# Optimization experiments

Hardware: AMD Instinct MI355X
Metric: run time of the kernel (lower is better)

## Reference

```python
import jax, jax.numpy as jnp
import numpy as np

LOSS_WEIGHT = 1.0
INTENSITY_WEIGHT = 0.5


def setup_inputs() -> dict:
    key = jax.random.key(0)
    k1, k2 = jax.random.split(key)
    N, M = 20000, 20000
    adv_pc = jax.random.normal(k1, (N, 4), dtype=jnp.float32)
    ori_pc = jax.random.normal(k2, (M, 4), dtype=jnp.float32)
    return {"adv_pc": adv_pc, "ori_pc": ori_pc}


def reference(adv_pc, ori_pc):
    adv_xyz = adv_pc[:, :3]  # [N,3]
    ori_xyz = ori_pc[:, :3]  # [M,3]

    # Squared pairwise distances via |a|^2 + |b|^2 - 2 a.b  -> [N,M]
    a2 = jnp.sum(adv_xyz * adv_xyz, axis=1)  # [N]
    b2 = jnp.sum(ori_xyz * ori_xyz, axis=1)  # [M]
    d2 = a2[:, None] + b2[None, :] - 2.0 * (adv_xyz @ ori_xyz.T)

    # 1-NN in both directions (knn_points with K=1 returns squared dists)
    min_dist_adv_to_ori = jnp.min(d2, axis=1)     # [N]
    adv_indices = jnp.argmin(d2, axis=1)          # [N] nearest ori for each adv
    min_dist_ori_to_adv = jnp.min(d2, axis=0)     # [M]
    ori_indices = jnp.argmin(d2, axis=0)          # [M] nearest adv for each ori

    chamfer_loss = jnp.mean(min_dist_adv_to_ori) + jnp.mean(min_dist_ori_to_adv)

    adv_intensity = adv_pc[:, 3]
    ori_intensity = ori_pc[:, 3]
    adv_intensity_diff_1 = jnp.mean((adv_intensity - ori_intensity[adv_indices]) ** 2)
    adv_intensity_diff_2 = jnp.mean((ori_intensity - adv_intensity[ori_indices]) ** 2)
    intensity_loss = (adv_intensity_diff_1 + adv_intensity_diff_2) / 2.0

    return chamfer_loss * LOSS_WEIGHT + intensity_loss * INTENSITY_WEIGHT
```

## Files before the change

### kernel.cpp

```cpp
#include <hip/hip_runtime.h>

#define CH 512
#define TPCH 16
#define QPB 256
#define YSL 8
#define RB 64

typedef __bf16 bf16x8 __attribute__((ext_vector_type(8)));
typedef float f32x16 __attribute__((ext_vector_type(16)));

__device__ __forceinline__ unsigned bfb(float x) {
    __bf16 h = (__bf16)x;
    return (unsigned)__builtin_bit_cast(unsigned short, h);
}
__device__ __forceinline__ float bff(unsigned b) {
    return (float)__builtin_bit_cast(__bf16, (unsigned short)b);
}

__device__ __forceinline__ void stage_one(uint4* a_lds, int local, float4 p, bool valid) {
    float x, y, z, u;
    if (valid) {
        x = p.x; y = p.y; z = p.z;
        u = 0.25f * fmaf(p.x, p.x, fmaf(p.y, p.y, p.z * p.z));
    } else {
        x = 0.f; y = 0.f; z = 0.f; u = 130.f;
    }
    unsigned xh = bfb(x); unsigned xl = bfb(x - bff(xh));
    unsigned yh = bfb(y); unsigned yl = bfb(y - bff(yh));
    unsigned zh = bfb(z); unsigned zl = bfb(z - bff(zh));
    unsigned uh = bfb(u); float u1 = u - bff(uh);
    unsigned ul = bfb(u1); unsigned ull = bfb(u1 - bff(ul));
    uint4 h0, h1;
    h0.x = xh | (xl << 16); h0.y = h0.x;
    h0.z = yh | (yl << 16); h0.w = h0.z;
    h1.x = zh | (zl << 16); h1.y = h1.x;
    h1.z = uh | (ul << 16);
    h1.w = ull | (0x43A0u << 16);
    int t = local >> 5, r = local & 31;
    a_lds[t * 64 + r]      = h0;
    a_lds[t * 64 + 32 + r] = h1;
}

__device__ __forceinline__ bf16x8 make_bfrag(float4 qp, int h) {
    float cx = -0.5f * qp.x, cy = -0.5f * qp.y, cz = -0.5f * qp.z;
    unsigned cxh = bfb(cx); unsigned cxl = bfb(cx - bff(cxh));
    unsigned cyh = bfb(cy); unsigned cyl = bfb(cy - bff(cyh));
    unsigned czh = bfb(cz); unsigned czl = bfb(cz - bff(czh));
    uint4 braw;
    if (h == 0) {
        braw.x = cxh | (cxh << 16); braw.y = cxl | (cxl << 16);
        braw.z = cyh | (cyh << 16); braw.w = cyl | (cyl << 16);
    } else {
        braw.x = czh | (czh << 16); braw.y = czl | (czl << 16);
        braw.z = 0x3F803F80u;       braw.w = 0x3F803F80u;
    }
    return __builtin_bit_cast(bf16x8, braw);
}

__device__ __forceinline__ void reduce_fold(const f32x16& acc, unsigned tl, unsigned& cm) {
    unsigned u0 = min(min(__float_as_uint(acc[0]),  __float_as_uint(acc[1])),  __float_as_uint(acc[2]));
    unsigned u1 = min(min(__float_as_uint(acc[3]),  __float_as_uint(acc[4])),  __float_as_uint(acc[5]));
    unsigned u2 = min(min(__float_as_uint(acc[6]),  __float_as_uint(acc[7])),  __float_as_uint(acc[8]));
    unsigned u3 = min(min(__float_as_uint(acc[9]),  __float_as_uint(acc[10])), __float_as_uint(acc[11]));
    unsigned u4 = min(min(__float_as_uint(acc[12]), __float_as_uint(acc[13])), __float_as_uint(acc[14]));
    unsigned u5 = min(min(u0, u1), u2);
    unsigned u6 = min(min(u3, u4), __float_as_uint(acc[15]));
    unsigned m  = min(u5, u6);
    cm = min(cm, (m << 9) | tl);
}

__global__ __launch_bounds__(256, 4) void mfma_nn(
    const float4* __restrict__ adv, int N,
    const float4* __restrict__ ori, int M,
    unsigned long long* __restrict__ slots, int S,
    int chunks)
{
    const int dir = blockIdx.z;
    const float4* __restrict__ q = dir ? ori : adv;
    const float4* __restrict__ t = dir ? adv : ori;
    const int nq = dir ? M : N;
    const int nt = dir ? N : M;
    unsigned long long* __restrict__ outrow =
        slots + (size_t)(dir * YSL + blockIdx.y) * (size_t)S;

    const int tid = threadIdx.x;
    const int wave = tid >> 6;
    const int lane = tid & 63;
    const int col = lane & 31;
    const int h = lane >> 5;

    const int qiA = blockIdx.x * QPB + wave * 32 + col;
    const int qiB = qiA + 128;
    const bool qvA = qiA < nq;
    const bool qvB = qiB < nq;
    float4 qpA = qvA ? q[qiA] : make_float4(0.f, 0.f, 0.f, 0.f);
    float4 qpB = qvB ? q[qiB] : make_float4(0.f, 0.f, 0.f, 0.f);

    const bf16x8 bfragA = make_bfrag(qpA, h);
    const bf16x8 bfragB = make_bfrag(qpB, h);

    __shared__ uint4 a_lds[TPCH * 64];
    const f32x16 zero = {};

    const int slicebase = blockIdx.y * chunks * CH;
    unsigned cmA = 0xFFFFFFFFu;
    unsigned cmB = 0xFFFFFFFFu;
    int base = slicebase;

    for (int c = 0; c < chunks; ++c) {
        if (c) __syncthreads();
        {
            int j0 = base + tid, j1 = j0 + 256;
            if (base + CH <= nt) {
                stage_one(a_lds, tid,       t[j0], true);
                stage_one(a_lds, tid + 256, t[j1], true);
            } else {
                bool v0 = j0 < nt, v1 = j1 < nt;
                float4 p0 = v0 ? t[j0] : make_float4(0.f, 0.f, 0.f, 0.f);
                float4 p1 = v1 ? t[j1] : make_float4(0.f, 0.f, 0.f, 0.f);
                stage_one(a_lds, tid,       p0, v0);
                stage_one(a_lds, tid + 256, p1, v1);
            }
        }
        __syncthreads();

        const unsigned tl0 = (unsigned)(c << 4);
        #pragma unroll
        for (int tt = 0; tt < TPCH; ++tt) {
            bf16x8 a = __builtin_bit_cast(bf16x8, a_lds[tt * 64 + lane]);
            f32x16 acc0 = __builtin_amdgcn_mfma_f32_32x32x16_bf16(a, bfragA, zero, 0, 0, 0);
            reduce_fold(acc0, tl0 + (unsigned)tt, cmA);
            f32x16 acc1 = __builtin_amdgcn_mfma_f32_32x32x16_bf16(a, bfragB, zero, 0, 0, 0);
            reduce_fold(acc1, tl0 + (unsigned)tt, cmB);
        }
        base += CH;
    }

    #pragma unroll
    for (int s = 0; s < 2; ++s) {
        const unsigned cm = s ? cmB : cmA;
        const float4 qp  = s ? qpB : qpA;
        const int    qi  = s ? qiB : qiA;
        const bool   qv  = s ? qvB : qvA;
        const int jb = slicebase + (int)(cm & 0x7Fu) * 32 + 4 * h;
        unsigned long long run = 0xFFFFFFFFFFFFFFFFull;
        #pragma unroll
        for (int e = 0; e < 16; ++e) {
            int r = (e & 3) + ((e >> 2) << 3);
            int j = jb + r;
            if (j < nt) {
                float4 b = t[j];
                float dx = qp.x - b.x, dy = qp.y - b.y, dz = qp.z - b.z;
                float d2 = fmaf(dx, dx, fmaf(dy, dy, dz * dz));
                unsigned long long cand =
                    ((unsigned long long)__float_as_uint(d2) << 32) | (unsigned)j;
                run = cand < run ? cand : run;
            }
        }
        unsigned long long other = __shfl_xor(run, 32);
        run = run < other ? run : other;
        if (h == 0 && qv) outrow[qi] = run;
    }
}

__device__ inline float block_reduce_sum(float v, float* lds) {
    #pragma unroll
    for (int off = 32; off > 0; off >>= 1) v += __shfl_down(v, off, 64);
    int wave = threadIdx.x >> 6;
    int lane = threadIdx.x & 63;
    __syncthreads();
    if (lane == 0) lds[wave] = v;
    __syncthreads();
    float r = 0.f;
    if (threadIdx.x == 0) {
        #pragma unroll
        for (int w = 0; w < 4; ++w) r += lds[w];
    }
    return r;
}

__global__ __launch_bounds__(256) void partial_finalize(
    const unsigned long long* __restrict__ slots, int S,
    int n, int m,
    const float4* __restrict__ adv, const float4* __restrict__ ori,
    float* __restrict__ partials)
{
    __shared__ float lds[4];
    float s_min0 = 0.f, s_i1 = 0.f, s_min1 = 0.f, s_i2 = 0.f;
    const int stride = RB * 256;
    const int t0 = blockIdx.x * 256 + threadIdx.x;
    const unsigned long long* __restrict__ s0 = slots;
    const unsigned long long* __restrict__ s1 = slots + (size_t)YSL * S;

    for (int i = t0; i < n; i += stride) {
        unsigned long long k = s0[i];
        #pragma unroll
        for (int y = 1; y < YSL; ++y) k = min(k, s0[(size_t)y * S + i]);
        int j = (int)(unsigned int)(k & 0xFFFFFFFFu);
        s_min0 += __uint_as_float((unsigned int)(k >> 32));
        float dw = adv[i].w - ori[j].w;
        s_i1 += dw * dw;
    }
    for (int jj = t0; jj < m; jj += stride) {
        unsigned long long k = s1[jj];
        #pragma unroll
        for (int y = 1; y < YSL; ++y) k = min(k, s1[(size_t)y * S + jj]);
        int i = (int)(unsigned int)(k & 0xFFFFFFFFu);
        s_min1 += __uint_as_float((unsigned int)(k >> 32));
        float dw = ori[jj].w - adv[i].w;
        s_i2 += dw * dw;
    }

    float r0 = block_reduce_sum(s_min0, lds);
    float r1 = block_reduce_sum(s_i1, lds);
    float r2 = block_reduce_sum(s_min1, lds);
    float r3 = block_reduce_sum(s_i2, lds);

    if (threadIdx.x == 0) {
        partials[blockIdx.x * 4 + 0] = r0;
        partials[blockIdx.x * 4 + 1] = r1;
        partials[blockIdx.x * 4 + 2] = r2;
        partials[blockIdx.x * 4 + 3] = r3;
    }
}

__global__ __launch_bounds__(256) void combine(
    const float* __restrict__ partials, int n, int m, float* __restrict__ out)
{
    __shared__ float lds[4];
    float v0 = 0.f, v1 = 0.f, v2 = 0.f, v3 = 0.f;
    if (threadIdx.x < RB) {
        v0 = partials[threadIdx.x * 4 + 0];
        v1 = partials[threadIdx.x * 4 + 1];
        v2 = partials[threadIdx.x * 4 + 2];
        v3 = partials[threadIdx.x * 4 + 3];
    }
    float r0 = block_reduce_sum(v0, lds);
    float r1 = block_reduce_sum(v1, lds);
    float r2 = block_reduce_sum(v2, lds);
    float r3 = block_reduce_sum(v3, lds);
    if (threadIdx.x == 0) {
        float chamfer   = r0 / (float)n + r2 / (float)m;
        float intensity = 0.5f * (r1 / (float)n + r3 / (float)m);
        out[0] = chamfer * 1.0f + intensity * 0.5f;
    }
}

extern "C" void kernel_launch(void* const* d_in, const int* in_sizes, int n_in,
                              void* d_out, int out_size, void* d_ws, size_t ws_size,
                              hipStream_t stream) {
    const float4* adv = (const float4*)d_in[0];
    const float4* ori = (const float4*)d_in[1];
    const int N = in_sizes[0] / 4;
    const int M = in_sizes[1] / 4;
    const int S = max(N, M);

    unsigned long long* slots = (unsigned long long*)d_ws;
    float* partials = (float*)(slots + (size_t)2 * YSL * S);
    float* out = (float*)d_out;

    const int chunks = (S + YSL * CH - 1) / (YSL * CH);
    dim3 grid((S + QPB - 1) / QPB, YSL, 2);
    mfma_nn<<<grid, 256, 0, stream>>>(adv, N, ori, M, slots, S, chunks);

    partial_finalize<<<RB, 256, 0, stream>>>(slots, S, N, M, adv, ori, partials);
    combine<<<1, 256, 0, stream>>>(partials, N, M, out);
}
```

Baseline: 47.32 us.

## Precompute bf16 split fragments in a prep kernel and stream them from global memory

Adds a prep kernel that converts both point clouds once into the hi/lo bf16 MFMA A-fragment layout in workspace. The main kernel then loads each fragment straight from global memory (L2-resident) per lane, with no LDS staging and no __syncthreads. This removes the per-block redundant conversion work and the barriers between chunks. In exchange it adds one extra kernel launch, extra workspace, and puts global load latency directly in the MFMA loop, with only an unroll of 4 to hide it.

New measurement: 62.76 us. +32.6%, slower.

```diff
diff --git a/kernel.cpp b/kernel.cpp
--- a/kernel.cpp
+++ b/kernel.cpp
@@ -1,7 +1,6 @@
 #include <hip/hip_runtime.h>
 
 #define CH 512
-#define TPCH 16
 #define QPB 256
 #define YSL 8
 #define RB 64
@@ -17,7 +16,7 @@
     return (float)__builtin_bit_cast(__bf16, (unsigned short)b);
 }
 
-__device__ __forceinline__ void stage_one(uint4* a_lds, int local, float4 p, bool valid) {
+__device__ __forceinline__ void make_frag(float4 p, bool valid, uint4& h0, uint4& h1) {
     float x, y, z, u;
     if (valid) {
         x = p.x; y = p.y; z = p.z;
@@ -30,15 +29,30 @@
     unsigned zh = bfb(z); unsigned zl = bfb(z - bff(zh));
     unsigned uh = bfb(u); float u1 = u - bff(uh);
     unsigned ul = bfb(u1); unsigned ull = bfb(u1 - bff(ul));
-    uint4 h0, h1;
     h0.x = xh | (xl << 16); h0.y = h0.x;
     h0.z = yh | (yl << 16); h0.w = h0.z;
     h1.x = zh | (zl << 16); h1.y = h1.x;
     h1.z = uh | (ul << 16);
     h1.w = ull | (0x43A0u << 16);
-    int t = local >> 5, r = local & 31;
-    a_lds[t * 64 + r]      = h0;
-    a_lds[t * 64 + 32 + r] = h1;
+}
+
+__global__ __launch_bounds__(256) void prep(
+    const float4* __restrict__ adv, int N,
+    const float4* __restrict__ ori, int M,
+    uint4* __restrict__ frag0,
+    uint4* __restrict__ frag1,
+    int padded)
+{
+    int p = blockIdx.x * 256 + threadIdx.x;
+    if (p >= padded) return;
+    int base = (p >> 5) * 64 + (p & 31);
+    uint4 h0, h1;
+    bool v0 = p < M;
+    make_frag(v0 ? ori[p] : make_float4(0.f,0.f,0.f,0.f), v0, h0, h1);
+    frag0[base] = h0; frag0[base + 32] = h1;
+    bool v1 = p < N;
+    make_frag(v1 ? adv[p] : make_float4(0.f,0.f,0.f,0.f), v1, h0, h1);
+    frag1[base] = h0; frag1[base + 32] = h1;
 }
 
 __device__ __forceinline__ bf16x8 make_bfrag(float4 qp, int h) {
@@ -72,14 +86,17 @@
 __global__ __launch_bounds__(256, 4) void mfma_nn(
     const float4* __restrict__ adv, int N,
     const float4* __restrict__ ori, int M,
+    const uint4* __restrict__ frag0,
+    const uint4* __restrict__ frag1,
     unsigned long long* __restrict__ slots, int S,
-    int chunks)
+    int ntiles)
 {
     const int dir = blockIdx.z;
     const float4* __restrict__ q = dir ? ori : adv;
     const float4* __restrict__ t = dir ? adv : ori;
     const int nq = dir ? M : N;
     const int nt = dir ? N : M;
+    const uint4* __restrict__ frag = dir ? frag1 : frag0;
     unsigned long long* __restrict__ outrow =
         slots + (size_t)(dir * YSL + blockIdx.y) * (size_t)S;
 
@@ -98,42 +115,21 @@
 
     const bf16x8 bfragA = make_bfrag(qpA, h);
     const bf16x8 bfragB = make_bfrag(qpB, h);
-
-    __shared__ uint4 a_lds[TPCH * 64];
     const f32x16 zero = {};
 
-    const int slicebase = blockIdx.y * chunks * CH;
+    const int slicebase = blockIdx.y * ntiles * 32;
+    const uint4* __restrict__ fr = frag + (size_t)(slicebase >> 5) * 64 + lane;
+
     unsigned cmA = 0xFFFFFFFFu;
     unsigned cmB = 0xFFFFFFFFu;
-    int base = slicebase;
-
-    for (int c = 0; c < chunks; ++c) {
-        if (c) __syncthreads();
-        {
-            int j0 = base + tid, j1 = j0 + 256;
-            if (base + CH <= nt) {
-                stage_one(a_lds, tid,       t[j0], true);
-                stage_one(a_lds, tid + 256, t[j1], true);
-            } else {
-                bool v0 = j0 < nt, v1 = j1 < nt;
-                float4 p0 = v0 ? t[j0] : make_float4(0.f, 0.f, 0.f, 0.f);
-                float4 p1 = v1 ? t[j1] : make_float4(0.f, 0.f, 0.f, 0.f);
-                stage_one(a_lds, tid,       p0, v0);
-                stage_one(a_lds, tid + 256, p1, v1);
-            }
-        }
-        __syncthreads();
-
-        const unsigned tl0 = (unsigned)(c << 4);
-        #pragma unroll
-        for (int tt = 0; tt < TPCH; ++tt) {
-            bf16x8 a = __builtin_bit_cast(bf16x8, a_lds[tt * 64 + lane]);
-            f32x16 acc0 = __builtin_amdgcn_mfma_f32_32x32x16_bf16(a, bfragA, zero, 0, 0, 0);
-            reduce_fold(acc0, tl0 + (unsigned)tt, cmA);
-            f32x16 acc1 = __builtin_amdgcn_mfma_f32_32x32x16_bf16(a, bfragB, zero, 0, 0, 0);
-            reduce_fold(acc1, tl0 + (unsigned)tt, cmB);
-        }
-        base += CH;
+
+    #pragma unroll 4
+    for (int tl = 0; tl < ntiles; ++tl) {
+        bf16x8 a = __builtin_bit_cast(bf16x8, fr[(size_t)tl * 64]);
+        f32x16 acc0 = __builtin_amdgcn_mfma_f32_32x32x16_bf16(a, bfragA, zero, 0, 0, 0);
+        reduce_fold(acc0, (unsigned)tl, cmA);
+        f32x16 acc1 = __builtin_amdgcn_mfma_f32_32x32x16_bf16(a, bfragB, zero, 0, 0, 0);
+        reduce_fold(acc1, (unsigned)tl, cmB);
     }
 
     #pragma unroll
@@ -255,13 +251,20 @@
     const int M = in_sizes[1] / 4;
     const int S = max(N, M);
 
+    const int chunks = (S + YSL * CH - 1) / (YSL * CH);
+    const int ntiles = chunks * (CH / 32);
+    const int padded = YSL * ntiles * 32;
+
     unsigned long long* slots = (unsigned long long*)d_ws;
-    float* partials = (float*)(slots + (size_t)2 * YSL * S);
+    uint4* frag0 = (uint4*)(slots + (size_t)2 * YSL * S);
+    uint4* frag1 = frag0 + (size_t)padded * 2;
+    float* partials = (float*)(frag1 + (size_t)padded * 2);
     float* out = (float*)d_out;
 
-    const int chunks = (S + YSL * CH - 1) / (YSL * CH);
+    prep<<<(padded + 255) / 256, 256, 0, stream>>>(adv, N, ori, M, frag0, frag1, padded);
+
     dim3 grid((S + QPB - 1) / QPB, YSL, 2);
-    mfma_nn<<<grid, 256, 0, stream>>>(adv, N, ori, M, slots, S, chunks);
+    mfma_nn<<<grid, 256, 0, stream>>>(adv, N, ori, M, frag0, frag1, slots, S, ntiles);
 
     partial_finalize<<<RB, 256, 0, stream>>>(slots, S, N, M, adv, ori, partials);
     combine<<<1, 256, 0, stream>>>(partials, N, M, out);
```

## Stage targets per wave in private LDS and block four query groups per lane

Applied to the files above, without the earlier changes.

Each wave now loads and converts its own 256-target chunk into a private LDS region, which removes the block-wide __syncthreads between staging and MFMA use. Each lane also holds four query fragments instead of two, and the block covers 512 queries, so each loaded A fragment feeds four MFMAs. In exchange, every wave redundantly loads and converts the same targets, so conversion work per MFMA roughly doubles. Register pressure also rises and the grid has half as many blocks, which may lower occupancy.

Result: slower. 61.65 us (+30.3%).

```diff
diff --git a/kernel.cpp b/kernel.cpp
--- a/kernel.cpp
+++ b/kernel.cpp
@@ -1,8 +1,8 @@
 #include <hip/hip_runtime.h>
 
-#define CH 512
-#define TPCH 16
-#define QPB 256
+#define WCH 256
+#define WTPC 8
+#define QPB 512
 #define YSL 8
 #define RB 64
 
@@ -17,7 +17,7 @@
     return (float)__builtin_bit_cast(__bf16, (unsigned short)b);
 }
 
-__device__ __forceinline__ void stage_one(uint4* a_lds, int local, float4 p, bool valid) {
+__device__ __forceinline__ void make_frag(float4 p, bool valid, uint4& h0, uint4& h1) {
     float x, y, z, u;
     if (valid) {
         x = p.x; y = p.y; z = p.z;
@@ -30,15 +30,11 @@
     unsigned zh = bfb(z); unsigned zl = bfb(z - bff(zh));
     unsigned uh = bfb(u); float u1 = u - bff(uh);
     unsigned ul = bfb(u1); unsigned ull = bfb(u1 - bff(ul));
-    uint4 h0, h1;
     h0.x = xh | (xl << 16); h0.y = h0.x;
     h0.z = yh | (yl << 16); h0.w = h0.z;
     h1.x = zh | (zl << 16); h1.y = h1.x;
     h1.z = uh | (ul << 16);
     h1.w = ull | (0x43A0u << 16);
-    int t = local >> 5, r = local & 31;
-    a_lds[t * 64 + r]      = h0;
-    a_lds[t * 64 + 32 + r] = h1;
 }
 
 __device__ __forceinline__ bf16x8 make_bfrag(float4 qp, int h) {
@@ -73,7 +69,7 @@
     const float4* __restrict__ adv, int N,
     const float4* __restrict__ ori, int M,
     unsigned long long* __restrict__ slots, int S,
-    int chunks)
+    int wchunks)
 {
     const int dir = blockIdx.z;
     const float4* __restrict__ q = dir ? ori : adv;
@@ -89,59 +85,61 @@
     const int col = lane & 31;
     const int h = lane >> 5;
 
-    const int qiA = blockIdx.x * QPB + wave * 32 + col;
-    const int qiB = qiA + 128;
-    const bool qvA = qiA < nq;
-    const bool qvB = qiB < nq;
-    float4 qpA = qvA ? q[qiA] : make_float4(0.f, 0.f, 0.f, 0.f);
-    float4 qpB = qvB ? q[qiB] : make_float4(0.f, 0.f, 0.f, 0.f);
-
-    const bf16x8 bfragA = make_bfrag(qpA, h);
-    const bf16x8 bfragB = make_bfrag(qpB, h);
-
-    __shared__ uint4 a_lds[TPCH * 64];
+    const int qi0 = blockIdx.x * QPB + wave * 32 + col;
+    float4 qp[4]; bool qv[4]; bf16x8 bfrag[4];
+    #pragma unroll
+    for (int s = 0; s < 4; ++s) {
+        int qi = qi0 + s * 128;
+        qv[s] = qi < nq;
+        qp[s] = qv[s] ? q[qi] : make_float4(0.f, 0.f, 0.f, 0.f);
+        bfrag[s] = make_bfrag(qp[s], h);
+    }
     const f32x16 zero = {};
 
-    const int slicebase = blockIdx.y * chunks * CH;
-    unsigned cmA = 0xFFFFFFFFu;
-    unsigned cmB = 0xFFFFFFFFu;
+    __shared__ uint4 lds_all[4][WTPC * 64];
+    uint4* my_lds = lds_all[wave];
+
+    const int slicebase = blockIdx.y * wchunks * WCH;
+    unsigned cm0 = 0xFFFFFFFFu, cm1 = 0xFFFFFFFFu;
+    unsigned cm2 = 0xFFFFFFFFu, cm3 = 0xFFFFFFFFu;
     int base = slicebase;
 
-    for (int c = 0; c < chunks; ++c) {
-        if (c) __syncthreads();
+    for (int c = 0; c < wchunks; ++c) {
         {
-            int j0 = base + tid, j1 = j0 + 256;
-            if (base + CH <= nt) {
-                stage_one(a_lds, tid,       t[j0], true);
-                stage_one(a_lds, tid + 256, t[j1], true);
-            } else {
-                bool v0 = j0 < nt, v1 = j1 < nt;
-                float4 p0 = v0 ? t[j0] : make_float4(0.f, 0.f, 0.f, 0.f);
-                float4 p1 = v1 ? t[j1] : make_float4(0.f, 0.f, 0.f, 0.f);
-                stage_one(a_lds, tid,       p0, v0);
-                stage_one(a_lds, tid + 256, p1, v1);
+            bool full = (base + WCH <= nt);
+            #pragma unroll
+            for (int k = 0; k < 4; ++k) {
+                int j = base + k * 64 + lane;
+                bool v = full || (j < nt);
+                float4 p = v ? t[j] : make_float4(0.f, 0.f, 0.f, 0.f);
+                uint4 h0, h1;
+                make_frag(p, v, h0, h1);
+                int local = k * 64 + lane;
+                int tl = local >> 5, r = local & 31;
+                my_lds[tl * 64 + r]      = h0;
+                my_lds[tl * 64 + 32 + r] = h1;
             }
         }
-        __syncthreads();
-
-        const unsigned tl0 = (unsigned)(c << 4);
-        #pragma unroll
-        for (int tt = 0; tt < TPCH; ++tt) {
-            bf16x8 a = __builtin_bit_cast(bf16x8, a_lds[tt * 64 + lane]);
-            f32x16 acc0 = __builtin_amdgcn_mfma_f32_32x32x16_bf16(a, bfragA, zero, 0, 0, 0);
-            reduce_fold(acc0, tl0 + (unsigned)tt, cmA);
-            f32x16 acc1 = __builtin_amdgcn_mfma_f32_32x32x16_bf16(a, bfragB, zero, 0, 0, 0);
-            reduce_fold(acc1, tl0 + (unsigned)tt, cmB);
+
+        const unsigned tl0 = (unsigned)(c << 3);
+        #pragma unroll
+        for (int tt = 0; tt < WTPC; ++tt) {
+            bf16x8 a = __builtin_bit_cast(bf16x8, my_lds[tt * 64 + lane]);
+            f32x16 acc0 = __builtin_amdgcn_mfma_f32_32x32x16_bf16(a, bfrag[0], zero, 0, 0, 0);
+            reduce_fold(acc0, tl0 + (unsigned)tt, cm0);
+            f32x16 acc1 = __builtin_amdgcn_mfma_f32_32x32x16_bf16(a, bfrag[1], zero, 0, 0, 0);
+            reduce_fold(acc1, tl0 + (unsigned)tt, cm1);
+            f32x16 acc2 = __builtin_amdgcn_mfma_f32_32x32x16_bf16(a, bfrag[2], zero, 0, 0, 0);
+            reduce_fold(acc2, tl0 + (unsigned)tt, cm2);
+            f32x16 acc3 = __builtin_amdgcn_mfma_f32_32x32x16_bf16(a, bfrag[3], zero, 0, 0, 0);
+            reduce_fold(acc3, tl0 + (unsigned)tt, cm3);
         }
-        base += CH;
+        base += WCH;
     }
 
     #pragma unroll
-    for (int s = 0; s < 2; ++s) {
-        const unsigned cm = s ? cmB : cmA;
-        const float4 qp  = s ? qpB : qpA;
-        const int    qi  = s ? qiB : qiA;
-        const bool   qv  = s ? qvB : qvA;
+    for (int s = 0; s < 4; ++s) {
+        const unsigned cm = (s == 0) ? cm0 : (s == 1) ? cm1 : (s == 2) ? cm2 : cm3;
         const int jb = slicebase + (int)(cm & 0x7Fu) * 32 + 4 * h;
         unsigned long long run = 0xFFFFFFFFFFFFFFFFull;
         #pragma unroll
@@ -150,7 +148,7 @@
             int j = jb + r;
             if (j < nt) {
                 float4 b = t[j];
-                float dx = qp.x - b.x, dy = qp.y - b.y, dz = qp.z - b.z;
+                float dx = qp[s].x - b.x, dy = qp[s].y - b.y, dz = qp[s].z - b.z;
                 float d2 = fmaf(dx, dx, fmaf(dy, dy, dz * dz));
                 unsigned long long cand =
                     ((unsigned long long)__float_as_uint(d2) << 32) | (unsigned)j;
@@ -159,7 +157,7 @@
         }
         unsigned long long other = __shfl_xor(run, 32);
         run = run < other ? run : other;
-        if (h == 0 && qv) outrow[qi] = run;
+        if (h == 0 && qv[s]) outrow[qi0 + s * 128] = run;
     }
 }
 
@@ -259,9 +257,9 @@
     float* partials = (float*)(slots + (size_t)2 * YSL * S);
     float* out = (float*)d_out;
 
-    const int chunks = (S + YSL * CH - 1) / (YSL * CH);
+    const int wchunks = (S + YSL * WCH - 1) / (YSL * WCH);
     dim3 grid((S + QPB - 1) / QPB, YSL, 2);
-    mfma_nn<<<grid, 256, 0, stream>>>(adv, N, ori, M, slots, S, chunks);
+    mfma_nn<<<grid, 256, 0, stream>>>(adv, N, ori, M, slots, S, wchunks);
 
     partial_finalize<<<RB, 256, 0, stream>>>(slots, S, N, M, adv, ori, partials);
     combine<<<1, 256, 0, stream>>>(partials, N, M, out);
```
